# Optimization experiments

Measured on AMD Instinct MI355X. Metric: run time of the kernel, lower is better.

Reference implementation:

```python
import jax, jax.numpy as jnp
from jax import lax
import numpy as np

B, C, S, H, DH, DV, DW = 16, 256, 64, 8, 32, 32, 32  # batch, channels, input_size, heads, d_h, d_v, d_w


def _dwconv(x, w, b):
    # depthwise 3x3 conv, stride 1, pad 1. w: [C,1,3,3]
    y = lax.conv_general_dilated(x, w, (1, 1), ((1, 1), (1, 1)),
                                 dimension_numbers=('NCHW', 'OIHW', 'NCHW'),
                                 feature_group_count=x.shape[1])
    return y + b[None, :, None, None]


def _linear(x, w, b):
    # torch Linear: w [out,in]
    return x @ w.T + b


def setup_inputs() -> dict:
    key = jax.random.key(0)
    ks = jax.random.split(key, 26)
    n = lambda k, shape, s=0.02: jax.random.normal(k, shape, jnp.float32) * s
    conv = lambda k: n(k, (C, 1, 3, 3), 0.1)
    return {
        'x': jax.random.normal(ks[0], (B, C, S, S), jnp.float32),
        'dw_qh_w': conv(ks[1]), 'dw_qh_b': n(ks[2], (C,)),
        'fc_qh_w': n(ks[3], (H * DH, C)), 'fc_qh_b': n(ks[4], (H * DH,)),
        'dw_kh_w': conv(ks[5]), 'dw_kh_b': n(ks[6], (C,)),
        'fc_kh_w': n(ks[7], (H * DH, C)), 'fc_kh_b': n(ks[8], (H * DH,)),
        'Bh': n(ks[9], (1, H, S, S)),
        'dw_v_w': conv(ks[10]), 'dw_v_b': n(ks[11], (C,)),
        'fc_v_w': n(ks[12], (H * DV, C)), 'fc_v_b': n(ks[13], (H * DV,)),
        'dw_qw_w': conv(ks[14]), 'dw_qw_b': n(ks[15], (C,)),
        'fc_qw_w': n(ks[16], (H * DW, C)), 'fc_qw_b': n(ks[17], (H * DW,)),
        'dw_kw_w': conv(ks[18]), 'dw_kw_b': n(ks[19], (C,)),
        'fc_kw_w': n(ks[20], (H * DW, C)), 'fc_kw_b': n(ks[21], (H * DW,)),
        'Bw': n(ks[22], (1, H, S, S)),
        'fc_o_w': n(ks[23], (C, H * DV)), 'fc_o_b': n(ks[24], (C,)),
    }


def reference(x, dw_qh_w, dw_qh_b, fc_qh_w, fc_qh_b,
              dw_kh_w, dw_kh_b, fc_kh_w, fc_kh_b, Bh,
              dw_v_w, dw_v_b, fc_v_w, fc_v_b,
              dw_qw_w, dw_qw_b, fc_qw_w, fc_qw_b,
              dw_kw_w, dw_kw_b, fc_kw_w, fc_kw_b, Bw,
              fc_o_w, fc_o_b):
    b, c, h, w = x.shape
    sh = DH ** -0.5
    sw = DW ** -0.5

    # height-axis queries/keys: dwconv -> adaptive avg pool over width -> linear
    qh = _dwconv(x, dw_qh_w, dw_qh_b).mean(axis=3).transpose(0, 2, 1)  # [b,h,c]
    qh = _linear(qh, fc_qh_w, fc_qh_b).reshape(b, h, H, DH).transpose(0, 2, 1, 3)  # [b,H,h,dh]
    kh = _dwconv(x, dw_kh_w, dw_kh_b).mean(axis=3).transpose(0, 2, 1)
    kh = _linear(kh, fc_kh_w, fc_kh_b).reshape(b, h, H, DH).transpose(0, 2, 1, 3)
    attn_h = jax.nn.softmax(jnp.einsum('bhid,bhjd->bhij', qh, kh) * sh + Bh, axis=-1)  # [b,H,h,h]

    # values over full HxW grid
    v = _dwconv(x, dw_v_w, dw_v_b).reshape(b, c, h * w).transpose(0, 2, 1)  # [b,hw,c]
    v = _linear(v, fc_v_w, fc_v_b).reshape(b, h, w, H, DV).transpose(0, 3, 1, 2, 4)  # [b,H,h,w,dv]
    v = v.reshape(b, H, h, w * DV)

    # width-axis queries/keys: dwconv -> adaptive avg pool over height -> linear
    qw = _dwconv(x, dw_qw_w, dw_qw_b).mean(axis=2).transpose(0, 2, 1)  # [b,w,c]
    qw = _linear(qw, fc_qw_w, fc_qw_b).reshape(b, w, H, DW).transpose(0, 2, 1, 3)  # [b,H,w,dw]
    kw = _dwconv(x, dw_kw_w, dw_kw_b).mean(axis=2).transpose(0, 2, 1)
    kw = _linear(kw, fc_kw_w, fc_kw_b).reshape(b, w, H, DW).transpose(0, 2, 1, 3)
    attn_w = jax.nn.softmax(jnp.einsum('bhid,bhjd->bhij', qw, kw) * sw + Bw, axis=-1)  # [b,H,w,w]

    # dual axial mixing: height attention, then width attention
    r = jnp.matmul(attn_h, v)                                # [b,H,h,w*dv]
    r = r.reshape(b, H, h, w, DV).transpose(0, 1, 2, 4, 3)    # [b,H,h,dv,w]
    r = r.reshape(b, H, h * DV, w)
    r = jnp.matmul(r, attn_w)                                # [b,H,h*dv,w]
    r = r.reshape(b, H, h, DV, w).transpose(0, 2, 4, 1, 3)    # [b,h,w,H,dv]
    r = r.reshape(b, h * w, H * DV)
    out = _linear(r, fc_o_w, fc_o_b).reshape(b, C, h, w)      # faithful to torch .view
    return out
```

## Files before the change

kernel.cpp:

```cpp
#include <hip/hip_runtime.h>
#include <hip/hip_bf16.h>

typedef float f4v __attribute__((ext_vector_type(4)));
typedef short s8v __attribute__((ext_vector_type(8)));
typedef unsigned short u8v __attribute__((ext_vector_type(8)));

__device__ __forceinline__ float bf2f(ushort u) {
  union { unsigned int i; float f; } c; c.i = ((unsigned int)u) << 16;
  return c.f;
}
__device__ __forceinline__ ushort f2bf(float f) {
  union { ushort s; __hip_bfloat16 h; } c; c.h = __float2bfloat16(f);
  return c.s;
}

__global__ __launch_bounds__(256) void k_prep(const float* __restrict__ w0,
                                              const float* __restrict__ w1,
                                              const float* __restrict__ w2,
                                              const float* __restrict__ w3,
                                              const float* __restrict__ wv,
                                              const float* __restrict__ wo,
                                              float* __restrict__ wt,
                                              ushort* __restrict__ wbf) {
  int bx = blockIdx.x;
  int tid = threadIdx.x;
  if (bx < 1024) {
    int mat = bx >> 8, o = bx & 255;
    const float* p = mat == 0 ? w0 : mat == 1 ? w1 : mat == 2 ? w2 : w3;
    wt[(size_t)mat * 65536 + (size_t)tid * 256 + o] = p[o * 256 + tid];
  } else {
    int idx = (bx - 1024) * 256 + tid;
    const float* src = (idx >> 16) ? wo : wv;
    wbf[idx] = f2bf(src[idx & 65535]);
  }
}

__global__ __launch_bounds__(256) void k_conv(
    const float* __restrict__ x,
    const float* __restrict__ wqh, const float* __restrict__ bqh,
    const float* __restrict__ wkh, const float* __restrict__ bkh,
    const float* __restrict__ wv,  const float* __restrict__ bv,
    const float* __restrict__ wqw, const float* __restrict__ bqw,
    const float* __restrict__ wkw, const float* __restrict__ bkw,
    ushort* __restrict__ convV,
    float* __restrict__ qhm, float* __restrict__ khm,
    float* __restrict__ qwm, float* __restrict__ kwm) {
  __shared__ float xs[68 * 68];
  __shared__ float wl[5][9];
  __shared__ float bl[5];

  int bx = blockIdx.x;
  int b = bx >> 8;
  int c = bx & 255;
  int tid = threadIdx.x;
  int lane = tid & 63, wave = tid >> 6;

  const float* xp = x + (size_t)(b * 256 + c) * 4096;
#pragma unroll
  for (int i = 0; i < 4; i++) {
    int flat = tid + i * 256;
    int r = flat >> 4, c4 = (flat & 15) * 4;
    float4 v = *(const float4*)(xp + r * 64 + c4);
    *(float4*)&xs[(r + 1) * 68 + 4 + c4] = v;
  }
  if (tid < 72) { xs[tid] = 0.f; xs[65 * 68 + tid] = 0.f; }
  if (tid >= 72 && tid < 200) {
    int t = tid - 72;
    int pr = (t & 63) + 1, side = t >> 6;
    xs[pr * 68 + (side ? 68 : 3)] = 0.f;
  }
  if (tid >= 200 && tid < 245) {
    int t = tid - 200;
    int cw = t / 9, wi = t % 9;
    const float* wp = cw == 0 ? wqh : cw == 1 ? wkh : cw == 2 ? wv
                    : cw == 3 ? wqw : wkw;
    wl[cw][wi] = wp[c * 9 + wi];
  } else if (tid >= 245 && tid < 250) {
    int cw = tid - 245;
    const float* bp = cw == 0 ? bqh : cw == 1 ? bkh : cw == 2 ? bv
                    : cw == 3 ? bqw : bkw;
    bl[cw] = bp[c];
  }
  __syncthreads();

  {
    int w = lane;
    int h0 = wave * 16;
    float v0 = wl[2][0], v1 = wl[2][1], v2 = wl[2][2];
    float v3 = wl[2][3], v4 = wl[2][4], v5 = wl[2][5];
    float v6 = wl[2][6], v7 = wl[2][7], v8 = wl[2][8];
    float bvv = bl[2];
    float a00 = xs[h0 * 68 + 3 + w], a01 = xs[h0 * 68 + 4 + w],
          a02 = xs[h0 * 68 + 5 + w];
    float a10 = xs[(h0 + 1) * 68 + 3 + w], a11 = xs[(h0 + 1) * 68 + 4 + w],
          a12 = xs[(h0 + 1) * 68 + 5 + w];
    ushort* cp = convV + (size_t)(b * 256 + c) * 4096 + h0 * 64 + w;
#pragma unroll
    for (int i = 0; i < 16; i++) {
      int pr = h0 + i + 2;
      float a20 = xs[pr * 68 + 3 + w];
      float a21 = xs[pr * 68 + 4 + w];
      float a22 = xs[pr * 68 + 5 + w];
      float acc = bvv;
      acc += a00 * v0 + a01 * v1 + a02 * v2;
      acc += a10 * v3 + a11 * v4 + a12 * v5;
      acc += a20 * v6 + a21 * v7 + a22 * v8;
      cp[i * 64] = f2bf(acc);
      a00 = a10; a01 = a11; a02 = a12;
      a10 = a20; a11 = a21; a12 = a22;
    }
  }

  if (wave == 0) {
    float rs = 0.f, e0 = 0.f, e1 = 0.f;
    const float* rowp = &xs[(lane + 1) * 68 + 4];
#pragma unroll
    for (int i = 0; i < 16; i++) {
      float4 v = *(const float4*)(rowp + i * 4);
      rs += (v.x + v.y) + (v.z + v.w);
      if (i == 0) e0 = v.x;
      if (i == 15) e1 = v.w;
    }
    float rsP = __shfl(rs, lane - 1, 64); rsP = (lane == 0) ? 0.f : rsP;
    float rsN = __shfl(rs, lane + 1, 64); rsN = (lane == 63) ? 0.f : rsN;
    float e0P = __shfl(e0, lane - 1, 64); e0P = (lane == 0) ? 0.f : e0P;
    float e0N = __shfl(e0, lane + 1, 64); e0N = (lane == 63) ? 0.f : e0N;
    float e1P = __shfl(e1, lane - 1, 64); e1P = (lane == 0) ? 0.f : e1P;
    float e1N = __shfl(e1, lane + 1, 64); e1N = (lane == 63) ? 0.f : e1N;
    float RS[3] = {rsP, rs, rsN};
    float E0[3] = {e0P, e0, e0N};
    float E1[3] = {e1P, e1, e1N};
    float vq = 0.f, vk = 0.f;
#pragma unroll
    for (int ky = 0; ky < 3; ky++) {
      vq += (wl[0][ky * 3] + wl[0][ky * 3 + 1] + wl[0][ky * 3 + 2]) * RS[ky]
            - wl[0][ky * 3] * E1[ky] - wl[0][ky * 3 + 2] * E0[ky];
      vk += (wl[1][ky * 3] + wl[1][ky * 3 + 1] + wl[1][ky * 3 + 2]) * RS[ky]
            - wl[1][ky * 3] * E1[ky] - wl[1][ky * 3 + 2] * E0[ky];
    }
    qhm[(size_t)(b * 256 + c) * 64 + lane] = vq * (1.f / 64.f) + bl[0];
    khm[(size_t)(b * 256 + c) * 64 + lane] = vk * (1.f / 64.f) + bl[1];
  } else if (wave == 1) {
    float cs = 0.f, f0 = 0.f, f1 = 0.f;
#pragma unroll
    for (int r = 0; r < 64; r++) {
      float v = xs[(r + 1) * 68 + 4 + lane];
      cs += v;
      if (r == 0) f0 = v;
      if (r == 63) f1 = v;
    }
    float csP = __shfl(cs, lane - 1, 64); csP = (lane == 0) ? 0.f : csP;
    float csN = __shfl(cs, lane + 1, 64); csN = (lane == 63) ? 0.f : csN;
    float f0P = __shfl(f0, lane - 1, 64); f0P = (lane == 0) ? 0.f : f0P;
    float f0N = __shfl(f0, lane + 1, 64); f0N = (lane == 63) ? 0.f : f0N;
    float f1P = __shfl(f1, lane - 1, 64); f1P = (lane == 0) ? 0.f : f1P;
    float f1N = __shfl(f1, lane + 1, 64); f1N = (lane == 63) ? 0.f : f1N;
    float CS[3] = {csP, cs, csN};
    float F0[3] = {f0P, f0, f0N};
    float F1[3] = {f1P, f1, f1N};
    float vq = 0.f, vk = 0.f;
#pragma unroll
    for (int kx = 0; kx < 3; kx++) {
      vq += (wl[3][kx] + wl[3][3 + kx] + wl[3][6 + kx]) * CS[kx]
            - wl[3][kx] * F1[kx] - wl[3][6 + kx] * F0[kx];
      vk += (wl[4][kx] + wl[4][3 + kx] + wl[4][6 + kx]) * CS[kx]
            - wl[4][kx] * F1[kx] - wl[4][6 + kx] * F0[kx];
    }
    qwm[(size_t)(b * 256 + c) * 64 + lane] = vq * (1.f / 64.f) + bl[3];
    kwm[(size_t)(b * 256 + c) * 64 + lane] = vk * (1.f / 64.f) + bl[4];
  }
}

template <int OUT_BF16, int AT>
__global__ __launch_bounds__(256) void k_mm(const ushort* __restrict__ A,
                                            const ushort* __restrict__ W,
                                            const float* __restrict__ bias,
                                            void* __restrict__ out) {
  __shared__ __align__(16) ushort As[128 * 40];
  __shared__ __align__(16) ushort Bs[128 * 40];

  int m0 = blockIdx.x * 128;
  int n0 = blockIdx.y * 128;
  int tid = threadIdx.x;
  int lane = tid & 63, wave = tid >> 6;
  int wm = (wave & 1) * 64, wn = (wave >> 1) * 64;
  int tm = lane & 15, quad = lane >> 4;

  const ushort* Abase;
  if (AT) {
    Abase = A + (size_t)(m0 >> 12) * (256 * 4096) + (m0 & 4095);
  } else {
    Abase = A + (size_t)m0 * 256;
  }

  f4v acc[4][4] = {};

  for (int kc = 0; kc < 256; kc += 32) {
    __syncthreads();
    if (AT) {
      int kr2 = (tid & 15) * 2, mg = tid >> 4;
      u8v v0 = *(const u8v*)&Abase[(size_t)(kc + kr2) * 4096 + mg * 8];
      u8v v1 = *(const u8v*)&Abase[(size_t)(kc + kr2 + 1) * 4096 + mg * 8];
#pragma unroll
      for (int j = 0; j < 8; j++) {
        ushort pr[2] = {v0[j], v1[j]};
        *(uint*)&As[(mg * 8 + j) * 40 + kr2] = *(uint*)pr;
      }
#pragma unroll
      for (int h = 0; h < 2; h++) {
        int ch = tid + h * 256;
        int mr = ch >> 2, k8 = (ch & 3) * 8;
        *(float4*)&Bs[mr * 40 + k8] =
            *(const float4*)&W[(size_t)(n0 + mr) * 256 + kc + k8];
      }
    } else {
#pragma unroll
      for (int h = 0; h < 2; h++) {
        int ch = tid + h * 256;
        int mr = ch >> 2, k8 = (ch & 3) * 8;
        *(float4*)&As[mr * 40 + k8] =
            *(const float4*)&Abase[(size_t)mr * 256 + kc + k8];
        *(float4*)&Bs[mr * 40 + k8] =
            *(const float4*)&W[(size_t)(n0 + mr) * 256 + kc + k8];
      }
    }
    __syncthreads();

    s8v a[4], bfr[4];
#pragma unroll
    for (int mi = 0; mi < 4; mi++)
      a[mi] = *(const s8v*)&As[(wm + mi * 16 + tm) * 40 + quad * 8];
#pragma unroll
    for (int ni = 0; ni < 4; ni++)
      bfr[ni] = *(const s8v*)&Bs[(wn + ni * 16 + tm) * 40 + quad * 8];
#pragma unroll
    for (int mi = 0; mi < 4; mi++)
#pragma unroll
      for (int ni = 0; ni < 4; ni++)
        acc[mi][ni] = __builtin_amdgcn_mfma_f32_16x16x32_bf16(
            a[mi], bfr[ni], acc[mi][ni], 0, 0, 0);
  }

#pragma unroll
  for (int mi = 0; mi < 4; mi++) {
#pragma unroll
    for (int ni = 0; ni < 4; ni++) {
      int col = n0 + wn + ni * 16 + tm;
      float bv = bias[col];
#pragma unroll
      for (int r = 0; r < 4; r++) {
        int row = m0 + wm + mi * 16 + quad * 4 + r;
        float v = acc[mi][ni][r] + bv;
        if (OUT_BF16)
          ((ushort*)out)[(size_t)row * 256 + col] = f2bf(v);
        else
          ((float*)out)[(size_t)row * 256 + col] = v;
      }
    }
  }
}

__global__ __launch_bounds__(256) void k_gemm4(
    const float* __restrict__ s0, const float* __restrict__ s1,
    const float* __restrict__ s2, const float* __restrict__ s3,
    const float* __restrict__ wt,
    const float* __restrict__ b0, const float* __restrict__ b1,
    const float* __restrict__ b2, const float* __restrict__ b3,
    float* __restrict__ d0, float* __restrict__ d1,
    float* __restrict__ d2, float* __restrict__ d3) {
  __shared__ __align__(16) float As[32 * 64];
  __shared__ __align__(16) float Ws[32 * 64];

  int z = blockIdx.z;
  const float* At = z == 0 ? s0 : z == 1 ? s1 : z == 2 ? s2 : s3;
  const float* Wt = wt + (size_t)z * 65536;
  const float* bias = z == 0 ? b0 : z == 1 ? b1 : z == 2 ? b2 : b3;
  float* Cout = z == 0 ? d0 : z == 1 ? d1 : z == 2 ? d2 : d3;

  int m0 = blockIdx.x * 64;
  int n0 = blockIdx.y * 64;
  int tid = threadIdx.x;
  const float* Ab = At + (size_t)(m0 >> 6) * 256 * 64;

  int tx = tid & 15, ty = tid >> 4;
  int lk = tid >> 6;
  int lm = tid & 63;
  float acc[4][4] = {};

  for (int kc = 0; kc < 256; kc += 32) {
    __syncthreads();
#pragma unroll
    for (int r = 0; r < 8; r++) {
      int kk = lk + r * 4;
      As[kk * 64 + lm] = Ab[(size_t)(kc + kk) * 64 + lm];
      Ws[kk * 64 + lm] = Wt[(kc + kk) * 256 + n0 + lm];
    }
    __syncthreads();
#pragma unroll
    for (int kk = 0; kk < 32; kk++) {
      float4 av = *(const float4*)&As[kk * 64 + ty * 4];
      float4 wv = *(const float4*)&Ws[kk * 64 + tx * 4];
      float a_[4] = {av.x, av.y, av.z, av.w};
      float w_[4] = {wv.x, wv.y, wv.z, wv.w};
#pragma unroll
      for (int ii = 0; ii < 4; ii++)
#pragma unroll
        for (int jj = 0; jj < 4; jj++) acc[ii][jj] += a_[ii] * w_[jj];
    }
  }

#pragma unroll
  for (int ii = 0; ii < 4; ii++) {
    int m = m0 + ty * 4 + ii;
#pragma unroll
    for (int jj = 0; jj < 4; jj++) {
      int n = n0 + tx * 4 + jj;
      Cout[(size_t)m * 256 + n] = acc[ii][jj] + bias[n];
    }
  }
}

__global__ __launch_bounds__(256) void k_attn(
    const float* __restrict__ qh, const float* __restrict__ kh,
    const float* __restrict__ Bh, float* __restrict__ ah,
    const float* __restrict__ qw, const float* __restrict__ kw,
    const float* __restrict__ Bw, float* __restrict__ aw, float scale) {
  __shared__ float qs[4][32];
  __shared__ float ks[64 * 33];

  int bx = blockIdx.x;
  int setw = bx >> 11;
  int rem = bx & 2047;
  int ig = rem & 15, hd = (rem >> 4) & 7, b = rem >> 7;
  int tid = threadIdx.x;
  int wave = tid >> 6, lane = tid & 63;
  int i = ig * 4 + wave;

  const float* q = setw ? qw : qh;
  const float* k = setw ? kw : kh;
  const float* Bb = setw ? Bw : Bh;
  float* attn = setw ? aw : ah;

  if (lane < 32) qs[wave][lane] = q[(size_t)(b * 64 + i) * 256 + hd * 32 + lane];
#pragma unroll
  for (int it = 0; it < 8; it++) {
    int f = tid + it * 256;
    int j = f >> 5, d = f & 31;
    ks[j * 33 + d] = k[(size_t)(b * 64 + j) * 256 + hd * 32 + d];
  }
  __syncthreads();

  int j = lane;
  float dot = 0.f;
#pragma unroll
  for (int d = 0; d < 32; d++) dot += qs[wave][d] * ks[j * 33 + d];
  float logit = dot * scale + Bb[(hd * 64 + i) * 64 + j];
  float mx = logit;
#pragma unroll
  for (int off = 32; off > 0; off >>= 1)
    mx = fmaxf(mx, __shfl_xor(mx, off, 64));
  float e = __expf(logit - mx);
  float sum = e;
#pragma unroll
  for (int off = 32; off > 0; off >>= 1) sum += __shfl_xor(sum, off, 64);
  attn[(size_t)((b * 8 + hd) * 64 + i) * 64 + j] = e / sum;
}

__global__ __launch_bounds__(256) void k_av(const float* __restrict__ attn,
                                            const ushort* __restrict__ vlin,
                                            ushort* __restrict__ r1) {
  __shared__ __align__(16) float As[64 * 65];
  __shared__ __align__(16) float Bs[64 * 64];

  int bx = blockIdx.x;
  int cc = bx & 31, hd = (bx >> 5) & 7, b = bx >> 8;
  int tid = threadIdx.x;
  int l = tid & 63, g = tid >> 6;

  const float* ap = attn + (size_t)(b * 8 + hd) * 4096;
#pragma unroll
  for (int r = 0; r < 16; r++) {
    int i = g + r * 4;
    As[l * 65 + i] = ap[i * 64 + l];
  }
  int colg0 = cc * 64;
#pragma unroll
  for (int r = 0; r < 8; r++) {
    int f = tid + r * 256;
    int j = f >> 5, p2 = f & 31;
    int colg = colg0 + p2 * 2;
    int w = colg >> 5, dv = colg & 31;
    uint u = *(const uint*)&vlin[(size_t)(b * 4096 + j * 64 + w) * 256 +
                                 hd * 32 + dv];
    Bs[j * 64 + p2 * 2] = bf2f((ushort)(u & 0xffff));
    Bs[j * 64 + p2 * 2 + 1] = bf2f((ushort)(u >> 16));
  }
  __syncthreads();

  int tx = tid & 15, ty = tid >> 4;
  float acc[4][4] = {};
  for (int j = 0; j < 64; j++) {
    float4 bv = *(const float4*)&Bs[j * 64 + tx * 4];
    float b_[4] = {bv.x, bv.y, bv.z, bv.w};
    float a_[4];
#pragma unroll
    for (int ii = 0; ii < 4; ii++) a_[ii] = As[j * 65 + ty * 4 + ii];
#pragma unroll
    for (int ii = 0; ii < 4; ii++)
#pragma unroll
      for (int jj = 0; jj < 4; jj++) acc[ii][jj] += a_[ii] * b_[jj];
  }

  ushort* rp = r1 + (size_t)(b * 8 + hd) * 64 * 2048;
#pragma unroll
  for (int ii = 0; ii < 4; ii++) {
    int row = ty * 4 + ii;
    ushort pk[4];
#pragma unroll
    for (int jj = 0; jj < 4; jj++) pk[jj] = f2bf(acc[ii][jj]);
    *(uint2*)&rp[(size_t)row * 2048 + colg0 + tx * 4] = *(uint2*)pk;
  }
}

__global__ __launch_bounds__(256) void k_rw(const ushort* __restrict__ r1,
                                            const float* __restrict__ attnw,
                                            ushort* __restrict__ yT) {
  __shared__ __align__(16) float rr[2048];
  __shared__ __align__(16) float aw[4096];

  int bx = blockIdx.x;
  int h = bx & 63, hd = (bx >> 6) & 7, b = bx >> 9;
  int tid = threadIdx.x;

  const uint* rp = (const uint*)(r1 + (size_t)((b * 8 + hd) * 64 + h) * 2048);
#pragma unroll
  for (int r = 0; r < 4; r++) {
    uint u = rp[tid + r * 256];
    rr[2 * (tid + r * 256)] = bf2f((ushort)(u & 0xffff));
    rr[2 * (tid + r * 256) + 1] = bf2f((ushort)(u >> 16));
  }
  const float* ap = attnw + (size_t)(b * 8 + hd) * 4096;
#pragma unroll
  for (int r = 0; r < 4; r++)
    *(float4*)&aw[4 * (tid + r * 256)] = *(const float4*)&ap[4 * (tid + r * 256)];
  __syncthreads();

  int wp = tid & 63;
  int dv0 = (tid >> 6) * 8;
  float acc[8] = {};
  for (int w = 0; w < 64; w++) {
    float a = aw[w * 64 + wp];
    float4 r4a = *(const float4*)&rr[w * 32 + dv0];
    float4 r4b = *(const float4*)&rr[w * 32 + dv0 + 4];
    float rv[8] = {r4a.x, r4a.y, r4a.z, r4a.w, r4b.x, r4b.y, r4b.z, r4b.w};
#pragma unroll
    for (int d = 0; d < 8; d++) acc[d] += a * rv[d];
  }

  ushort* yp = yT + (size_t)(b * 4096 + h * 64 + wp) * 256 + hd * 32 + dv0;
  ushort pk[8];
#pragma unroll
  for (int d = 0; d < 8; d++) pk[d] = f2bf(acc[d]);
  *(uint4*)yp = *(uint4*)pk;
}

extern "C" void kernel_launch(void* const* d_in, const int* in_sizes, int n_in,
                              void* d_out, int out_size, void* d_ws,
                              size_t ws_size, hipStream_t stream) {
  const float* x      = (const float*)d_in[0];
  const float* dwqh_w = (const float*)d_in[1];
  const float* dwqh_b = (const float*)d_in[2];
  const float* fcqh_w = (const float*)d_in[3];
  const float* fcqh_b = (const float*)d_in[4];
  const float* dwkh_w = (const float*)d_in[5];
  const float* dwkh_b = (const float*)d_in[6];
  const float* fckh_w = (const float*)d_in[7];
  const float* fckh_b = (const float*)d_in[8];
  const float* Bh     = (const float*)d_in[9];
  const float* dwv_w  = (const float*)d_in[10];
  const float* dwv_b  = (const float*)d_in[11];
  const float* fcv_w  = (const float*)d_in[12];
  const float* fcv_b  = (const float*)d_in[13];
  const float* dwqw_w = (const float*)d_in[14];
  const float* dwqw_b = (const float*)d_in[15];
  const float* fcqw_w = (const float*)d_in[16];
  const float* fcqw_b = (const float*)d_in[17];
  const float* dwkw_w = (const float*)d_in[18];
  const float* dwkw_b = (const float*)d_in[19];
  const float* fckw_w = (const float*)d_in[20];
  const float* fckw_b = (const float*)d_in[21];
  const float* Bw     = (const float*)d_in[22];
  const float* fco_w  = (const float*)d_in[23];
  const float* fco_b  = (const float*)d_in[24];

  char* base = (char*)d_ws;
  ushort* P1 = (ushort*)(base);
  ushort* P2 = (ushort*)(base + 33554432);
  ushort* P3 = (ushort*)(base + 67108864);
  float*  wt   = (float*)(base + 100663296);
  ushort* wv_bf = (ushort*)(base + 101711872);
  float* qhm = (float*)(base + 101974016);
  float* khm = qhm + 262144;
  float* qwm = khm + 262144;
  float* kwm = qwm + 262144;
  float* qhl = kwm + 262144;
  float* khl = qhl + 262144;
  float* qwl = khl + 262144;
  float* kwl = qwl + 262144;
  float* ah  = kwl + 262144;
  float* awt = ah + 524288;
  if (ws_size < 115000000ull) return;

  const float scale = 0.17677669529663687f;

  k_prep<<<1536, 256, 0, stream>>>(fcqh_w, fckh_w, fcqw_w, fckw_w, fcv_w,
                                   fco_w, wt, wv_bf);
  k_conv<<<4096, 256, 0, stream>>>(x, dwqh_w, dwqh_b, dwkh_w, dwkh_b, dwv_w,
                                   dwv_b, dwqw_w, dwqw_b, dwkw_w, dwkw_b, P1,
                                   qhm, khm, qwm, kwm);
  k_gemm4<<<dim3(16, 4, 4), 256, 0, stream>>>(qhm, khm, qwm, kwm, wt, fcqh_b,
                                              fckh_b, fcqw_b, fckw_b, qhl, khl,
                                              qwl, kwl);
  k_attn<<<4096, 256, 0, stream>>>(qhl, khl, Bh, ah, qwl, kwl, Bw, awt, scale);
  k_mm<1, 1><<<dim3(512, 2), 256, 0, stream>>>(P1, wv_bf, fcv_b, P3);
  k_av<<<4096, 256, 0, stream>>>(ah, P3, P1);
  k_rw<<<8192, 256, 0, stream>>>(P1, awt, P2);
  k_mm<0, 0><<<dim3(512, 2), 256, 0, stream>>>(P2, wv_bf + 65536, fco_b, d_out);
}
```

Baseline: 319.2 us.

## Rewrite width-attention mixing kernel with bf16 MFMA and split-precision weights

The width-axis attention product in k_rw moves from scalar FP32 FMAs to bf16 MFMA 16x16x32 instructions. The attention weights are split into hi and lo bf16 parts so precision stays close to FP32. Each block now handles 8 rows of h instead of 1, which reuses the loaded attention matrix across rows and cuts the grid from 8192 to 1024 blocks. The cost is transposing data into padded LDS and running twice as many MFMAs to cover the hi/lo split.

```diff
diff --git a/kernel.cpp b/kernel.cpp
--- a/kernel.cpp
+++ b/kernel.cpp
@@ -425,43 +425,104 @@
 __global__ __launch_bounds__(256) void k_rw(const ushort* __restrict__ r1,
                                             const float* __restrict__ attnw,
                                             ushort* __restrict__ yT) {
-  __shared__ __align__(16) float rr[2048];
-  __shared__ __align__(16) float aw[4096];
+  __shared__ __align__(16) ushort As[8 * 2180];
+  __shared__ __align__(16) ushort Wh[64 * 68];
+  __shared__ __align__(16) ushort Wl[64 * 68];
 
   int bx = blockIdx.x;
-  int h = bx & 63, hd = (bx >> 6) & 7, b = bx >> 9;
-  int tid = threadIdx.x;
-
-  const uint* rp = (const uint*)(r1 + (size_t)((b * 8 + hd) * 64 + h) * 2048);
-#pragma unroll
-  for (int r = 0; r < 4; r++) {
-    uint u = rp[tid + r * 256];
-    rr[2 * (tid + r * 256)] = bf2f((ushort)(u & 0xffff));
-    rr[2 * (tid + r * 256) + 1] = bf2f((ushort)(u >> 16));
-  }
-  const float* ap = attnw + (size_t)(b * 8 + hd) * 4096;
-#pragma unroll
-  for (int r = 0; r < 4; r++)
-    *(float4*)&aw[4 * (tid + r * 256)] = *(const float4*)&ap[4 * (tid + r * 256)];
+  int ht = bx & 7, hd = (bx >> 3) & 7, b = bx >> 6;
+  int tid = threadIdx.x;
+  int lane = tid & 63, wave = tid >> 6;
+
+  {
+    int h = tid >> 5;
+    int t = tid & 31;
+    const ushort* rp =
+        r1 + (size_t)((b * 8 + hd) * 64 + ht * 8 + h) * 2048;
+#pragma unroll
+    for (int i = 0; i < 4; i++) {
+      int chunk = t + 32 * i;
+      int w = (chunk >> 2) * 2;
+      int dv0 = (chunk & 3) * 8;
+      u8v v0 = *(const u8v*)&rp[w * 32 + dv0];
+      u8v v1 = *(const u8v*)&rp[(w + 1) * 32 + dv0];
+#pragma unroll
+      for (int j = 0; j < 8; j++) {
+        ushort pr[2] = {(ushort)v0[j], (ushort)v1[j]};
+        *(uint*)&As[h * 2180 + (dv0 + j) * 68 + w] = *(uint*)pr;
+      }
+    }
+  }
+  {
+    const float* ap = attnw + (size_t)(b * 8 + hd) * 4096;
+#pragma unroll
+    for (int p = 0; p < 4; p++) {
+      int w = (tid >> 4) + p * 16;
+      int wq = (tid & 15) * 4;
+      float4 v = *(const float4*)&ap[w * 64 + wq];
+      float f_[4] = {v.x, v.y, v.z, v.w};
+#pragma unroll
+      for (int j = 0; j < 4; j++) {
+        ushort hi = f2bf(f_[j]);
+        Wh[(wq + j) * 68 + w] = hi;
+        Wl[(wq + j) * 68 + w] = f2bf(f_[j] - bf2f(hi));
+      }
+    }
+  }
   __syncthreads();
 
-  int wp = tid & 63;
-  int dv0 = (tid >> 6) * 8;
-  float acc[8] = {};
-  for (int w = 0; w < 64; w++) {
-    float a = aw[w * 64 + wp];
-    float4 r4a = *(const float4*)&rr[w * 32 + dv0];
-    float4 r4b = *(const float4*)&rr[w * 32 + dv0 + 4];
-    float rv[8] = {r4a.x, r4a.y, r4a.z, r4a.w, r4b.x, r4b.y, r4b.z, r4b.w};
-#pragma unroll
-    for (int d = 0; d < 8; d++) acc[d] += a * rv[d];
-  }
-
-  ushort* yp = yT + (size_t)(b * 4096 + h * 64 + wp) * 256 + hd * 32 + dv0;
-  ushort pk[8];
-#pragma unroll
-  for (int d = 0; d < 8; d++) pk[d] = f2bf(acc[d]);
-  *(uint4*)yp = *(uint4*)pk;
+  int tm = lane & 15, quad = lane >> 4;
+  int h0 = wave * 2;
+  f4v acc[4][4] = {};
+#pragma unroll
+  for (int kc = 0; kc < 64; kc += 32) {
+    s8v a[4], bh[4], bl[4];
+#pragma unroll
+    for (int mi = 0; mi < 4; mi++) {
+      int h = h0 + (mi >> 1);
+      int dv = (mi & 1) * 16 + tm;
+      int idx = h * 2180 + dv * 68 + kc + quad * 8;
+      union { s8v v; unsigned long long u[2]; } t_;
+      t_.u[0] = *(const unsigned long long*)&As[idx];
+      t_.u[1] = *(const unsigned long long*)&As[idx + 4];
+      a[mi] = t_.v;
+    }
+#pragma unroll
+    for (int ni = 0; ni < 4; ni++) {
+      int idx = (ni * 16 + tm) * 68 + kc + quad * 8;
+      union { s8v v; unsigned long long u[2]; } th, tl;
+      th.u[0] = *(const unsigned long long*)&Wh[idx];
+      th.u[1] = *(const unsigned long long*)&Wh[idx + 4];
+      tl.u[0] = *(const unsigned long long*)&Wl[idx];
+      tl.u[1] = *(const unsigned long long*)&Wl[idx + 4];
+      bh[ni] = th.v;
+      bl[ni] = tl.v;
+    }
+#pragma unroll
+    for (int mi = 0; mi < 4; mi++)
+#pragma unroll
+      for (int ni = 0; ni < 4; ni++) {
+        acc[mi][ni] = __builtin_amdgcn_mfma_f32_16x16x32_bf16(
+            a[mi], bh[ni], acc[mi][ni], 0, 0, 0);
+        acc[mi][ni] = __builtin_amdgcn_mfma_f32_16x16x32_bf16(
+            a[mi], bl[ni], acc[mi][ni], 0, 0, 0);
+      }
+  }
+
+#pragma unroll
+  for (int mi = 0; mi < 4; mi++) {
+    int h = ht * 8 + h0 + (mi >> 1);
+    int dv0 = (mi & 1) * 16 + quad * 4;
+#pragma unroll
+    for (int ni = 0; ni < 4; ni++) {
+      int wp = ni * 16 + tm;
+      ushort pk[4];
+#pragma unroll
+      for (int r = 0; r < 4; r++) pk[r] = f2bf(acc[mi][ni][r]);
+      *(uint2*)&yT[(size_t)(b * 4096 + h * 64 + wp) * 256 + hd * 32 + dv0] =
+          *(uint2*)pk;
+    }
+  }
 }
 
 extern "C" void kernel_launch(void* const* d_in, const int* in_sizes, int n_in,
@@ -524,6 +585,6 @@
   k_attn<<<4096, 256, 0, stream>>>(qhl, khl, Bh, ah, qwl, kwl, Bw, awt, scale);
   k_mm<1, 1><<<dim3(512, 2), 256, 0, stream>>>(P1, wv_bf, fcv_b, P3);
   k_av<<<4096, 256, 0, stream>>>(ah, P3, P1);
-  k_rw<<<8192, 256, 0, stream>>>(P1, awt, P2);
+  k_rw<<<1024, 256, 0, stream>>>(P1, awt, P2);
   k_mm<0, 0><<<dim3(512, 2), 256, 0, stream>>>(P2, wv_bf + 65536, fco_b, d_out);
 }
```

Result: faster. 294.6 us (-7.7%).
